# Optimization experiments

Hardware: AMD Instinct MI355X
Metric: run time of the kernel (lower is better)

Reference implementation:

```python
import jax, jax.numpy as jnp
import numpy as np

T, B, E, H = 256, 8, 512, 32
EXP = 512            # number of expanded (periodic-image) keys
SMOOTH = 20.0        # smooth_factor


def setup_inputs() -> dict:
    key = jax.random.key(0)
    ks = jax.random.split(key, 12)
    s = 1.0 / np.sqrt(E)
    return {
        "query": jax.random.normal(ks[0], (T, B, E), dtype=jnp.float32),
        "outcell_index": jax.random.randint(ks[1], (B, EXP), 0, T),
        "expand_mask": jax.random.bernoulli(ks[2], 0.1, (B, EXP)),
        "key_padding_mask": jax.random.bernoulli(ks[3], 0.1, (B, T)),
        "local_attention_weight": jax.random.uniform(ks[4], (B, T, T + EXP), dtype=jnp.float32),
        "Wq": jax.random.normal(ks[5], (E, E), dtype=jnp.float32) * s,
        "bq": jnp.zeros((E,), dtype=jnp.float32),
        "Wk": jax.random.normal(ks[6], (E, E), dtype=jnp.float32) * s,   # k_bias=False
        "Wv": jax.random.normal(ks[7], (E, E), dtype=jnp.float32) * s,
        "bv": jnp.zeros((E,), dtype=jnp.float32),
        "Wo": jax.random.normal(ks[8], (E, E), dtype=jnp.float32) * s,
        "bo": jnp.zeros((E,), dtype=jnp.float32),
    }


def reference(query, outcell_index, expand_mask, key_padding_mask,
              local_attention_weight, Wq, bq, Wk, Wv, bv, Wo, bo):
    t, b, e = query.shape
    hd = e // H
    # QKV projections (torch Linear: y = x @ W.T + b)
    q = jnp.einsum('tbe,fe->tbf', query, Wq) + bq
    k = jnp.einsum('tbe,fe->tbf', query, Wk)          # no k bias
    v = jnp.einsum('tbe,fe->tbf', query, Wv) + bv
    # PBC gather-expand K/V along the time axis
    oc = outcell_index.T[:, :, None]                  # [EXP, B, 1]
    k = jnp.concatenate([k, jnp.take_along_axis(k, oc, axis=0)], axis=0)  # [S,B,E]
    v = jnp.concatenate([v, jnp.take_along_axis(v, oc, axis=0)], axis=0)
    s_len = k.shape[0]
    # [len, B, E] -> [B, H, len, hd]
    qh = q.reshape(t, b, H, hd).transpose(1, 2, 0, 3)
    kh = k.reshape(s_len, b, H, hd).transpose(1, 2, 0, 3)
    vh = v.reshape(s_len, b, H, hd).transpose(1, 2, 0, 3)
    # NOTE: forward() never applies self.scaling in this path (faithful)
    scores = jnp.einsum('bhtd,bhsd->bhts', qh, kh)    # [B,H,T,S]
    law = local_attention_weight[:, None]             # [B,1,T,S]
    scores = (scores + SMOOTH) * law - SMOOTH         # smooth softmax
    kpm = jnp.concatenate([key_padding_mask, expand_mask], axis=1)  # [B,S]
    scores = jnp.where(kpm[:, None, None, :], -jnp.inf, scores)
    probs = jax.nn.softmax(scores, axis=-1)
    probs = probs * law                               # post-softmax reweight
    attn = jnp.einsum('bhts,bhsd->bhtd', probs, vh)   # [B,H,T,hd]
    attn = attn.transpose(2, 0, 1, 3).reshape(t, b, e)
    return jnp.einsum('tbe,fe->tbf', attn, Wo) + bo
```

## Files before the change

### kernel.cpp

```cpp
#include <hip/hip_runtime.h>
#include <stdint.h>

#define T_ 256
#define B_ 8
#define E_ 512
#define H_ 32
#define HD_ 16
#define EXP_ 512
#define S_ 768
#define M_ 2048
#define SMOOTH_ 20.0f
#define PSTR 36
#define VSTR 800
#define OSTR 20

typedef __attribute__((ext_vector_type(8)))  short bf16x8;
typedef __attribute__((ext_vector_type(4)))  float f32x4;
typedef __attribute__((ext_vector_type(16))) float f32x16;

__device__ __forceinline__ unsigned int pk2(float a, float b)
{
    unsigned int ua = __float_as_uint(a);
    ua = ua + 0x7FFFu + ((ua >> 16) & 1u);
    unsigned int ub = __float_as_uint(b);
    ub = ub + 0x7FFFu + ((ub >> 16) & 1u);
    return (ua >> 16) | (ub & 0xFFFF0000u);
}
__device__ __forceinline__ ushort bf1(float a)
{
    unsigned int u = __float_as_uint(a);
    u = u + 0x7FFFu + ((u >> 16) & 1u);
    return (ushort)(u >> 16);
}

union U16 { uint4 u; bf16x8 v; };

__global__ __launch_bounds__(256)
void conv_kernel(const float* __restrict__ X,
                 const float* __restrict__ Wq, const float* __restrict__ Wk,
                 const float* __restrict__ Wv, const float* __restrict__ Wo,
                 ushort* __restrict__ Xb, ushort* __restrict__ Wb)
{
    const int seg = blockIdx.x >> 6;
    const int blk = blockIdx.x & 63;
    const float* src;
    ushort* dst;
    if (seg < 4) { src = X + (size_t)seg * 262144; dst = Xb + (size_t)seg * 262144; }
    else {
        const float* ws_[4] = {Wq, Wk, Wv, Wo};
        src = ws_[seg - 4];
        dst = Wb + (size_t)(seg - 4) * 262144;
    }
    const int base = blk * 4096 + threadIdx.x * 16;
    float4 f0 = *(const float4*)&src[base + 0];
    float4 f1 = *(const float4*)&src[base + 4];
    float4 f2 = *(const float4*)&src[base + 8];
    float4 f3 = *(const float4*)&src[base + 12];
    *(uint4*)&dst[base + 0] = make_uint4(pk2(f0.x, f0.y), pk2(f0.z, f0.w),
                                         pk2(f1.x, f1.y), pk2(f1.z, f1.w));
    *(uint4*)&dst[base + 8] = make_uint4(pk2(f2.x, f2.y), pk2(f2.z, f2.w),
                                         pk2(f3.x, f3.y), pk2(f3.z, f3.w));
}

__device__ __forceinline__ void mfma_gemm_body_bf(const ushort* __restrict__ Xr,
                                                  int xstep,
                                                  const ushort* __restrict__ Wr,
                                                  int wstep,
                                                  f32x4 acc[2][2],
                                                  ushort* As, ushort* Bs)
{
    const int tid  = threadIdx.x;
    const int lrow = tid >> 2;
    const int kq   = tid & 3;
    const int l    = tid & 63;
    const int w    = tid >> 6;
    const int wm   = w & 1;
    const int wn   = w >> 1;
    const int lq   = l >> 4;
    const int ln   = l & 15;

    ushort* Aw = &As[lrow * 72 + kq * 16];
    ushort* Bw = &Bs[lrow * 72 + kq * 16];

    uint4 a0 = *(const uint4*)&Xr[0];
    uint4 a1 = *(const uint4*)&Xr[8];
    uint4 b0 = *(const uint4*)&Wr[0];
    uint4 b1 = *(const uint4*)&Wr[8];

    for (int it = 0; it < E_ / 64; ++it) {
        __syncthreads();
        *(uint4*)&Aw[0] = a0;
        *(uint4*)&Aw[8] = a1;
        *(uint4*)&Bw[0] = b0;
        *(uint4*)&Bw[8] = b1;
        __syncthreads();
        if (it < E_ / 64 - 1) {
            Xr += xstep; Wr += wstep;
            a0 = *(const uint4*)&Xr[0];
            a1 = *(const uint4*)&Xr[8];
            b0 = *(const uint4*)&Wr[0];
            b1 = *(const uint4*)&Wr[8];
        }
#pragma unroll
        for (int kb = 0; kb < 2; ++kb) {
            bf16x8 af0 = *(const bf16x8*)&As[(32 * wm + ln) * 72 + 32 * kb + lq * 8];
            bf16x8 af1 = *(const bf16x8*)&As[(32 * wm + 16 + ln) * 72 + 32 * kb + lq * 8];
            bf16x8 bf0 = *(const bf16x8*)&Bs[(32 * wn + ln) * 72 + 32 * kb + lq * 8];
            bf16x8 bf1 = *(const bf16x8*)&Bs[(32 * wn + 16 + ln) * 72 + 32 * kb + lq * 8];
            acc[0][0] = __builtin_amdgcn_mfma_f32_16x16x32_bf16(af0, bf0, acc[0][0], 0, 0, 0);
            acc[0][1] = __builtin_amdgcn_mfma_f32_16x16x32_bf16(af0, bf1, acc[0][1], 0, 0, 0);
            acc[1][0] = __builtin_amdgcn_mfma_f32_16x16x32_bf16(af1, bf0, acc[1][0], 0, 0, 0);
            acc[1][1] = __builtin_amdgcn_mfma_f32_16x16x32_bf16(af1, bf1, acc[1][1], 0, 0, 0);
        }
    }
}

__global__ __launch_bounds__(256)
void qkv_gemm(const ushort* __restrict__ Xb, const ushort* __restrict__ Wb,
              const float* __restrict__ bq, const float* __restrict__ bv,
              ushort* __restrict__ Qb, ushort* __restrict__ Kb,
              ushort* __restrict__ Vb)
{
    __shared__ __align__(16) ushort AsBs[2 * 64 * 72];
    ushort* As = AsBs;
    ushort* Bs = AsBs + 64 * 72;

    const int z = blockIdx.z;
    const ushort* W    = Wb + (size_t)z * 262144;
    const float*  bias = (z == 0) ? bq : (z == 2 ? bv : nullptr);
    ushort* dst        = (z == 0) ? Qb : (z == 1 ? Kb : Vb);

    const int m0 = blockIdx.y * 64;
    const int n0 = blockIdx.x * 64;

    f32x4 acc[2][2];
#pragma unroll
    for (int i = 0; i < 2; ++i)
#pragma unroll
        for (int j = 0; j < 2; ++j)
            acc[i][j] = (f32x4){0.f, 0.f, 0.f, 0.f};

    const int tid  = threadIdx.x;
    const int lrow = tid >> 2;
    const int kq   = tid & 3;
    mfma_gemm_body_bf(&Xb[(size_t)(m0 + lrow) * E_ + kq * 16], 64,
                      &W[(size_t)(n0 + lrow) * E_ + kq * 16], 64,
                      acc, As, Bs);

    const int l  = tid & 63;
    const int w  = tid >> 6;
    const int wm = w & 1;
    const int wn = w >> 1;
    const int lq = l >> 4;
    const int ln = l & 15;

    const float b0_ = bias ? bias[n0 + 32 * wn + ln]      : 0.f;
    const float b1_ = bias ? bias[n0 + 32 * wn + 16 + ln] : 0.f;

    __syncthreads();
    ushort* Ls = As;
#pragma unroll
    for (int j = 0; j < 2; ++j) {
        const float bb = j ? b1_ : b0_;
#pragma unroll
        for (int i = 0; i < 2; ++i)
#pragma unroll
            for (int r = 0; r < 4; ++r)
                Ls[(32 * wm + 16 * i + lq * 4 + r) * 72 + 32 * wn + 16 * j + ln] =
                    bf1(acc[i][j][r] + bb);
    }
    __syncthreads();

    {
        const int lm = tid & 63;
        const int hh = tid >> 6;
        uint4 f0 = *(const uint4*)&Ls[lm * 72 + hh * 16];
        uint4 f1 = *(const uint4*)&Ls[lm * 72 + hh * 16 + 8];
        const int m = m0 + lm;
        const int t = m >> 3;
        const int b = m & 7;
        const int h = (n0 >> 4) + hh;
        ushort* dp = &dst[(((size_t)(b * H_ + h)) * T_ + t) * HD_];
        *(uint4*)&dp[0] = f0;
        *(uint4*)&dp[8] = f1;
    }
}

__global__ __launch_bounds__(256)
void out_gemm(const ushort* __restrict__ Ab, const ushort* __restrict__ Wob,
              const float* __restrict__ bo, float* __restrict__ dst)
{
    __shared__ __align__(16) ushort AsBs[2 * 64 * 72];
    ushort* As = AsBs;
    ushort* Bs = AsBs + 64 * 72;

    const int m0 = blockIdx.y * 64;
    const int n0 = blockIdx.x * 64;

    f32x4 acc[2][2];
#pragma unroll
    for (int i = 0; i < 2; ++i)
#pragma unroll
        for (int j = 0; j < 2; ++j)
            acc[i][j] = (f32x4){0.f, 0.f, 0.f, 0.f};

    const int tid  = threadIdx.x;
    const int lrow = tid >> 2;
    const int kq   = tid & 3;
    const int m    = m0 + lrow;
    const int t    = m >> 3;
    const int b    = m & 7;
    mfma_gemm_body_bf(&Ab[(((size_t)(b * H_ + kq)) * T_ + t) * HD_], 4 * T_ * HD_,
                      &Wob[(size_t)(n0 + lrow) * E_ + kq * 16], 64,
                      acc, As, Bs);

    const int l  = tid & 63;
    const int w  = tid >> 6;
    const int wm = w & 1;
    const int wn = w >> 1;
    const int lq = l >> 4;
    const int ln = l & 15;

    const float bo0 = bo[n0 + 32 * wn + ln];
    const float bo1 = bo[n0 + 32 * wn + 16 + ln];

    __syncthreads();
    float* Lf = (float*)AsBs;
#pragma unroll
    for (int j = 0; j < 2; ++j) {
        const float bb = j ? bo1 : bo0;
#pragma unroll
        for (int i = 0; i < 2; ++i)
#pragma unroll
            for (int r = 0; r < 4; ++r)
                Lf[(32 * wm + 16 * i + lq * 4 + r) * 68 + 32 * wn + 16 * j + ln] =
                    acc[i][j][r] + bb;
    }
    __syncthreads();

    {
        const int lm = tid & 63;
        const int hh = tid >> 6;
        float* dp = &dst[(size_t)(m0 + lm) * E_ + n0 + hh * 16];
#pragma unroll
        for (int c = 0; c < 4; ++c) {
            float4 v = *(const float4*)&Lf[lm * 68 + hh * 16 + c * 4];
            *(float4*)&dp[c * 4] = v;
        }
    }
}

__device__ __forceinline__ void scat8(ushort* d, uint4 u)
{
    d[0 * VSTR] = (ushort)(u.x);  d[1 * VSTR] = (ushort)(u.x >> 16);
    d[2 * VSTR] = (ushort)(u.y);  d[3 * VSTR] = (ushort)(u.y >> 16);
    d[4 * VSTR] = (ushort)(u.z);  d[5 * VSTR] = (ushort)(u.z >> 16);
    d[6 * VSTR] = (ushort)(u.w);  d[7 * VSTR] = (ushort)(u.w >> 16);
}

__global__ __launch_bounds__(512)
void attn_kernel(const ushort* __restrict__ Qb, const ushort* __restrict__ Kb,
                 const ushort* __restrict__ Vb, const float* __restrict__ LAW,
                 const int* __restrict__ kpm, const int* __restrict__ em,
                 const int* __restrict__ oc, ushort* __restrict__ Ab)
{
    __shared__ __align__(16) ushort Ks[S_ * HD_];
    __shared__ __align__(16) ushort Vt[HD_ * VSTR];
    __shared__ __align__(16) float  msf[S_];
    __shared__ __align__(16) ushort Pb[8][32 * PSTR];

    float* Obuf = (float*)Ks;
    float* Zb   = (float*)Ks + 128 * OSTR;
    ushort* Ob  = (ushort*)Pb;

    const int tid    = threadIdx.x;
    const int blk    = blockIdx.x;
    const int bh     = blk >> 1;
    const int thalf  = blk & 1;
    const int b      = bh >> 5;
    const int h      = bh & 31;

    ((uint4*)Ks)[tid] = ((const uint4*)&Kb[(size_t)bh * T_ * HD_])[tid];
    {
        const int t    = tid >> 1;
        const int half = tid & 1;
        uint4 v = *(const uint4*)&Vb[((size_t)bh * T_ + t) * HD_ + half * 8];
        scat8(&Vt[half * 8 * VSTR + t], v);
    }
    {
        const int j   = tid;
        const int src = oc[b * EXP_ + j];
        const uint4* kr = (const uint4*)&Kb[((size_t)bh * T_ + src) * HD_];
        *(uint4*)&Ks[(T_ + j) * HD_ + 0] = kr[0];
        *(uint4*)&Ks[(T_ + j) * HD_ + 8] = kr[1];
        const uint4* vr = (const uint4*)&Vb[((size_t)bh * T_ + src) * HD_];
        scat8(&Vt[T_ + j], vr[0]);
        scat8(&Vt[8 * VSTR + T_ + j], vr[1]);
    }
    {
        const int s = tid;
        const int m = (s < T_) ? kpm[b * T_ + s] : em[b * EXP_ + (s - T_)];
        msf[s] = m ? 0.f : 1.f;
        if (tid < 256) {
            const int s2 = 512 + tid;
            msf[s2] = em[b * EXP_ + (s2 - T_)] ? 0.f : 1.f;
        }
    }

    const int w      = tid >> 6;
    const int l      = tid & 63;
    const int tloc   = l & 31;
    const int khalf  = l >> 5;
    const int wt     = w & 3;
    const int sh     = w >> 2;
    const int tglob  = thalf * 128 + wt * 32 + tloc;
    bf16x8 qf = *(const bf16x8*)&Qb[((size_t)bh * T_ + tglob) * HD_ + khalf * 8];

    __syncthreads();

    const f32x16 zero16 = {0.f,0.f,0.f,0.f,0.f,0.f,0.f,0.f,
                           0.f,0.f,0.f,0.f,0.f,0.f,0.f,0.f};
    f32x4 o0 = {0.f, 0.f, 0.f, 0.f};
    f32x4 o1 = {0.f, 0.f, 0.f, 0.f};
    float Z = 0.f;

    const float* lawp = &LAW[((size_t)b * T_ + tglob) * S_];
    ushort* prow = &Pb[w][tloc * PSTR];
    const int tl = l & 15;
    const int kg = l >> 4;

    for (int i = sh * 12; i < sh * 12 + 12; ++i) {
        bf16x8 kf = *(const bf16x8*)&Ks[(i * 32 + tloc) * HD_ + khalf * 8];
        f32x16 sc = __builtin_amdgcn_mfma_f32_32x32x16_bf16(kf, qf, zero16, 0, 0, 0);

#pragma unroll
        for (int qd = 0; qd < 4; ++qd) {
            const int sb = i * 32 + qd * 8 + khalf * 4;
            float4 mf = *(const float4*)&msf[sb];
            float4 lw = *(const float4*)&lawp[sb];
            float e0, e1, e2, e3;
            {
                float x = (sc[qd*4+0] + SMOOTH_) * lw.x - SMOOTH_;
                e0 = mf.x * __expf(x - 50.f);
                x = (sc[qd*4+1] + SMOOTH_) * lw.y - SMOOTH_;
                e1 = mf.y * __expf(x - 50.f);
                x = (sc[qd*4+2] + SMOOTH_) * lw.z - SMOOTH_;
                e2 = mf.z * __expf(x - 50.f);
                x = (sc[qd*4+3] + SMOOTH_) * lw.w - SMOOTH_;
                e3 = mf.w * __expf(x - 50.f);
            }
            Z += (e0 + e1) + (e2 + e3);
            *(uint2*)&prow[qd * 8 + khalf * 4] =
                make_uint2(pk2(e0 * lw.x, e1 * lw.y), pk2(e2 * lw.z, e3 * lw.w));
        }

        bf16x8 vf = *(const bf16x8*)&Vt[tl * VSTR + i * 32 + kg * 8];
        {
            const ushort* pr0 = &Pb[w][(0 * 16 + tl) * PSTR + kg * 8];
            U16 u;
            uint2 a0 = *(const uint2*)pr0;
            uint2 a1 = *(const uint2*)(pr0 + 4);
            u.u = make_uint4(a0.x, a0.y, a1.x, a1.y);
            o0 = __builtin_amdgcn_mfma_f32_16x16x32_bf16(vf, u.v, o0, 0, 0, 0);
            const ushort* pr1 = &Pb[w][(1 * 16 + tl) * PSTR + kg * 8];
            uint2 b0 = *(const uint2*)pr1;
            uint2 b1 = *(const uint2*)(pr1 + 4);
            u.u = make_uint4(b0.x, b0.y, b1.x, b1.y);
            o1 = __builtin_amdgcn_mfma_f32_16x16x32_bf16(vf, u.v, o1, 0, 0, 0);
        }
    }

    Z += __shfl_xor(Z, 32);

    __syncthreads();

    if (sh == 1) {
#pragma unroll
        for (int th = 0; th < 2; ++th) {
            const f32x4 o = th ? o1 : o0;
            *(float4*)&Obuf[((wt * 2 + th) * 16 + tl) * OSTR + kg * 4] =
                make_float4(o[0], o[1], o[2], o[3]);
        }
        if (l < 32) Zb[wt * 32 + tloc] = Z;
    }
    __syncthreads();

    if (sh == 0) {
        const float Ztot = Z + Zb[wt * 32 + tloc];
#pragma unroll
        for (int th = 0; th < 2; ++th) {
            const float Zt  = __shfl(Ztot, th * 16 + tl);
            const float inv = (Zt > 0.f) ? 1.f / Zt : 0.f;
            float4 po = *(const float4*)&Obuf[((wt * 2 + th) * 16 + tl) * OSTR + kg * 4];
            const f32x4 o = th ? o1 : o0;
            const int trow = wt * 32 + th * 16 + tl;
            float ov[4] = {(o[0] + po.x) * inv, (o[1] + po.y) * inv,
                           (o[2] + po.z) * inv, (o[3] + po.w) * inv};
            *(uint*)&Ob[trow * 16 + kg * 4]     = pk2(ov[0], ov[1]);
            *(uint*)&Ob[trow * 16 + kg * 4 + 2] = pk2(ov[2], ov[3]);
        }
    }
    __syncthreads();

    if (tid < 256) {
        ushort* dp = &Ab[(((size_t)(b * H_ + h)) * T_ + thalf * 128) * HD_];
        *(uint4*)&dp[tid * 8] = *(const uint4*)&Ob[tid * 8];
    }
}

extern "C" void kernel_launch(void* const* d_in, const int* in_sizes, int n_in,
                              void* d_out, int out_size, void* d_ws, size_t ws_size,
                              hipStream_t stream)
{
    const float* query = (const float*)d_in[0];
    const int*   oc    = (const int*)d_in[1];
    const int*   em    = (const int*)d_in[2];
    const int*   kpm   = (const int*)d_in[3];
    const float* law   = (const float*)d_in[4];
    const float* Wq    = (const float*)d_in[5];
    const float* bq    = (const float*)d_in[6];
    const float* Wk    = (const float*)d_in[7];
    const float* Wv    = (const float*)d_in[8];
    const float* bv    = (const float*)d_in[9];
    const float* Wo    = (const float*)d_in[10];
    const float* bo    = (const float*)d_in[11];
    float* out = (float*)d_out;

    ushort* Xb  = (ushort*)d_ws;
    ushort* Wb  = Xb  + (size_t)1048576;
    ushort* Qb  = Wb  + (size_t)1048576;
    ushort* Kb  = Qb  + (size_t)1048576;
    ushort* Vb  = Kb  + (size_t)1048576;
    ushort* Ab  = Vb  + (size_t)1048576;

    conv_kernel<<<512, 256, 0, stream>>>(query, Wq, Wk, Wv, Wo, Xb, Wb);

    dim3 gq(E_ / 64, M_ / 64, 3);
    qkv_gemm<<<gq, 256, 0, stream>>>(Xb, Wb, bq, bv, Qb, Kb, Vb);

    attn_kernel<<<B_ * H_ * 2, 512, 0, stream>>>(Qb, Kb, Vb, law, kpm, em, oc, Ab);

    dim3 go(E_ / 64, M_ / 64, 1);
    out_gemm<<<go, 256, 0, stream>>>(Ab, Wb + (size_t)3 * 262144, bo, out);
}
```

Before: 129.2 us.

## Swap MFMA operand order so lanes index keys for coalesced LAW loads

Swaps the A/B operands of the score MFMA so each lane holds one key column and rows span queries. LAW is then read with consecutive lanes touching consecutive key positions, which gives coalesced scalar loads instead of per-lane float4 loads strided by rows. The trade-off is a per-row Z accumulator array reduced with 5x16 cross-lane shuffles, scalar 16-bit LDS stores for P, and a new Zpart shared buffer. The P stride is padded to 40 and the output staging moves to Vt.

Measured after the change: 126.5 us. -2.1%, faster.

```diff
diff --git a/kernel.cpp b/kernel.cpp
--- a/kernel.cpp
+++ b/kernel.cpp
@@ -10,7 +10,7 @@
 #define S_ 768
 #define M_ 2048
 #define SMOOTH_ 20.0f
-#define PSTR 36
+#define PSTR 40
 #define VSTR 800
 #define OSTR 20
 
@@ -268,10 +268,10 @@
     __shared__ __align__(16) ushort Vt[HD_ * VSTR];
     __shared__ __align__(16) float  msf[S_];
     __shared__ __align__(16) ushort Pb[8][32 * PSTR];
-
-    float* Obuf = (float*)Ks;
-    float* Zb   = (float*)Ks + 128 * OSTR;
-    ushort* Ob  = (ushort*)Pb;
+    __shared__ __align__(16) float  Zpart[2][128];
+
+    float*  Obuf = (float*)Ks;
+    ushort* Ob   = (ushort*)Vt;
 
     const int tid    = threadIdx.x;
     const int blk    = blockIdx.x;
@@ -309,12 +309,12 @@
 
     const int w      = tid >> 6;
     const int l      = tid & 63;
-    const int tloc   = l & 31;
+    const int slane  = l & 31;
     const int khalf  = l >> 5;
     const int wt     = w & 3;
     const int sh     = w >> 2;
-    const int tglob  = thalf * 128 + wt * 32 + tloc;
-    bf16x8 qf = *(const bf16x8*)&Qb[((size_t)bh * T_ + tglob) * HD_ + khalf * 8];
+    const int tbase  = thalf * 128 + wt * 32;
+    bf16x8 qf = *(const bf16x8*)&Qb[((size_t)bh * T_ + tbase + slane) * HD_ + khalf * 8];
 
     __syncthreads();
 
@@ -322,36 +322,33 @@
                            0.f,0.f,0.f,0.f,0.f,0.f,0.f,0.f};
     f32x4 o0 = {0.f, 0.f, 0.f, 0.f};
     f32x4 o1 = {0.f, 0.f, 0.f, 0.f};
-    float Z = 0.f;
-
-    const float* lawp = &LAW[((size_t)b * T_ + tglob) * S_];
-    ushort* prow = &Pb[w][tloc * PSTR];
+    float zacc[16];
+#pragma unroll
+    for (int r = 0; r < 16; ++r) zacc[r] = 0.f;
+
+    const float* lawb = &LAW[((size_t)b * T_ + tbase + khalf * 4) * S_ + slane];
+    ushort* pw = &Pb[w][slane];
     const int tl = l & 15;
     const int kg = l >> 4;
 
     for (int i = sh * 12; i < sh * 12 + 12; ++i) {
-        bf16x8 kf = *(const bf16x8*)&Ks[(i * 32 + tloc) * HD_ + khalf * 8];
-        f32x16 sc = __builtin_amdgcn_mfma_f32_32x32x16_bf16(kf, qf, zero16, 0, 0, 0);
-
-#pragma unroll
-        for (int qd = 0; qd < 4; ++qd) {
-            const int sb = i * 32 + qd * 8 + khalf * 4;
-            float4 mf = *(const float4*)&msf[sb];
-            float4 lw = *(const float4*)&lawp[sb];
-            float e0, e1, e2, e3;
-            {
-                float x = (sc[qd*4+0] + SMOOTH_) * lw.x - SMOOTH_;
-                e0 = mf.x * __expf(x - 50.f);
-                x = (sc[qd*4+1] + SMOOTH_) * lw.y - SMOOTH_;
-                e1 = mf.y * __expf(x - 50.f);
-                x = (sc[qd*4+2] + SMOOTH_) * lw.z - SMOOTH_;
-                e2 = mf.z * __expf(x - 50.f);
-                x = (sc[qd*4+3] + SMOOTH_) * lw.w - SMOOTH_;
-                e3 = mf.w * __expf(x - 50.f);
-            }
-            Z += (e0 + e1) + (e2 + e3);
-            *(uint2*)&prow[qd * 8 + khalf * 4] =
-                make_uint2(pk2(e0 * lw.x, e1 * lw.y), pk2(e2 * lw.z, e3 * lw.w));
+        bf16x8 kf = *(const bf16x8*)&Ks[(i * 32 + slane) * HD_ + khalf * 8];
+
+        float lw[16];
+        const float* lp = lawb + i * 32;
+#pragma unroll
+        for (int r = 0; r < 16; ++r)
+            lw[r] = lp[(size_t)((r & 3) + 8 * (r >> 2)) * S_];
+
+        f32x16 sc = __builtin_amdgcn_mfma_f32_32x32x16_bf16(qf, kf, zero16, 0, 0, 0);
+        const float mval = msf[i * 32 + slane];
+
+#pragma unroll
+        for (int r = 0; r < 16; ++r) {
+            const float x = (sc[r] + SMOOTH_) * lw[r] - SMOOTH_;
+            const float e = mval * __expf(x - 50.f);
+            zacc[r] += e;
+            pw[((r & 3) + 8 * (r >> 2) + 4 * khalf) * PSTR] = bf1(e * lw[r]);
         }
 
         bf16x8 vf = *(const bf16x8*)&Vt[tl * VSTR + i * 32 + kg * 8];
@@ -370,10 +367,20 @@
         }
     }
 
-    Z += __shfl_xor(Z, 32);
-
-    __syncthreads();
-
+#pragma unroll
+    for (int m = 1; m < 32; m <<= 1) {
+#pragma unroll
+        for (int r = 0; r < 16; ++r)
+            zacc[r] += __shfl_xor(zacc[r], m);
+    }
+
+    __syncthreads();
+
+    if (l == 0 || l == 32) {
+#pragma unroll
+        for (int r = 0; r < 16; ++r)
+            Zpart[sh][wt * 32 + (r & 3) + 8 * (r >> 2) + 4 * khalf] = zacc[r];
+    }
     if (sh == 1) {
 #pragma unroll
         for (int th = 0; th < 2; ++th) {
@@ -381,19 +388,17 @@
             *(float4*)&Obuf[((wt * 2 + th) * 16 + tl) * OSTR + kg * 4] =
                 make_float4(o[0], o[1], o[2], o[3]);
         }
-        if (l < 32) Zb[wt * 32 + tloc] = Z;
     }
     __syncthreads();
 
     if (sh == 0) {
-        const float Ztot = Z + Zb[wt * 32 + tloc];
 #pragma unroll
         for (int th = 0; th < 2; ++th) {
-            const float Zt  = __shfl(Ztot, th * 16 + tl);
+            const int trow = wt * 32 + th * 16 + tl;
+            const float Zt  = Zpart[0][trow] + Zpart[1][trow];
             const float inv = (Zt > 0.f) ? 1.f / Zt : 0.f;
             float4 po = *(const float4*)&Obuf[((wt * 2 + th) * 16 + tl) * OSTR + kg * 4];
             const f32x4 o = th ? o1 : o0;
-            const int trow = wt * 32 + th * 16 + tl;
             float ov[4] = {(o[0] + po.x) * inv, (o[1] + po.y) * inv,
                            (o[2] + po.z) * inv, (o[3] + po.w) * inv};
             *(uint*)&Ob[trow * 16 + kg * 4]     = pk2(ov[0], ov[1]);
```
